# Performance work log

Measured on AMD Instinct MI355X. Metric: run time of the kernel, lower is better.

Reference implementation:

```python
import jax, jax.numpy as jnp
import numpy as np

HIDDEN = 4096
NUM_HEADS = 32
HEAD_DIM = 128          # kv_channels
KV_GROUPS = 2           # multi_query_group_num
ROPE_BASE = 10000.0
ROPE_RATIO = 1.0
QKV_DIM = NUM_HEADS * HEAD_DIM + 2 * KV_GROUPS * HEAD_DIM  # 4608
T = 2048


def _rope_cache(positions):
    # build_rotary_pos with n_elem = rotary_dim//2 = 64 -> 32 frequencies
    n_elem = HEAD_DIM // 2
    theta = 1.0 / (ROPE_BASE ** (jnp.arange(0, n_elem, 2, dtype=jnp.float32) / n_elem))  # [32]
    idx_theta = (positions.astype(jnp.float32) / ROPE_RATIO)[:, None] * theta[None, :]   # [T,32]
    return jnp.cos(idx_theta), jnp.sin(idx_theta)


def _apply_rope(x, cos, sin):
    # x: [T, n_heads, HEAD_DIM]; first rot_dim=2*n_freq dims rotated in interleaved pairs
    t, n, _ = x.shape
    rot_dim = 2 * cos.shape[-1]  # 64
    x_rot, x_pass = x[..., :rot_dim], x[..., rot_dim:]
    xs = x_rot.reshape(t, n, rot_dim // 2, 2)
    c = cos[:, None, :]
    s = sin[:, None, :]
    o0 = xs[..., 0] * c - xs[..., 1] * s
    o1 = xs[..., 1] * c + xs[..., 0] * s
    out = jnp.stack([o0, o1], axis=-1).reshape(t, n, rot_dim)
    return jnp.concatenate([out, x_pass], axis=-1)


def setup_inputs() -> dict:
    key = jax.random.key(0)
    k1, k2, k3, k4 = jax.random.split(key, 4)
    return {
        "positions": jnp.arange(T, dtype=jnp.int64 if jax.config.jax_enable_x64 else jnp.int32),
        "hidden_states": jax.random.normal(k1, (T, HIDDEN), dtype=jnp.float32),
        "w_qkv": jax.random.normal(k2, (HIDDEN, QKV_DIM), dtype=jnp.float32) * 0.02,
        "b_qkv": jax.random.normal(k3, (QKV_DIM,), dtype=jnp.float32) * 0.02,
        "w_dense": jax.random.normal(k4, (HIDDEN, HIDDEN), dtype=jnp.float32) * 0.02,
    }


def reference(positions, hidden_states, w_qkv, b_qkv, w_dense):
    t = hidden_states.shape[0]
    qkv = hidden_states @ w_qkv + b_qkv  # [T, 4608]
    q_sz = NUM_HEADS * HEAD_DIM
    kv_sz = KV_GROUPS * HEAD_DIM
    q = qkv[:, :q_sz].reshape(t, NUM_HEADS, HEAD_DIM)
    k = qkv[:, q_sz:q_sz + kv_sz].reshape(t, KV_GROUPS, HEAD_DIM)
    v = qkv[:, q_sz + kv_sz:].reshape(t, KV_GROUPS, HEAD_DIM)

    cos, sin = _rope_cache(positions)
    q = _apply_rope(q, cos, sin)
    k = _apply_rope(k, cos, sin)

    rep = NUM_HEADS // KV_GROUPS  # MQA: repeat_interleave kv heads
    k = jnp.repeat(k, rep, axis=1)  # [T, NUM_HEADS, HEAD_DIM]
    v = jnp.repeat(v, rep, axis=1)

    scale = HEAD_DIM ** -0.5
    scores = jnp.einsum('qhd,khd->hqk', q, k) * scale  # [H, T, T]
    causal = positions[:, None] >= positions[None, :]
    scores = jnp.where(causal[None, :, :], scores, jnp.float32(-1e9))
    attn = jax.nn.softmax(scores, axis=-1)
    ctx = jnp.einsum('hqk,khd->qhd', attn, v).reshape(t, NUM_HEADS * HEAD_DIM)
    return ctx @ w_dense
```

## Files before the change

kernel.cpp:

```cpp
#include <hip/hip_runtime.h>
#include <hip/hip_bf16.h>

#define T_SEQ 2048
#define HIDDEN_SZ 4096
#define NUM_HEADS 32
#define HEAD_DIM 128
#define KV_GROUPS 2
#define Q_SZ 4096
#define KV_SZ 256
#define QKV_DIM 4608

typedef __attribute__((ext_vector_type(8))) short bf16x8_t;
typedef __attribute__((ext_vector_type(4))) float f32x4_t;

__device__ inline void store_c(float* p, float v) { *p = v; }
__device__ inline void store_c(__hip_bfloat16* p, float v) { *p = __float2bfloat16(v); }

#define GLDS16(gp, lp)                                                                  \
    __builtin_amdgcn_global_load_lds((const __attribute__((address_space(1))) unsigned int*)(gp), \
                                     (__attribute__((address_space(3))) unsigned int*)(lp), 16, 0, 0)

__global__ __launch_bounds__(256) void convert_bf16_kernel(const float* __restrict__ in,
                                                           __hip_bfloat16* __restrict__ out,
                                                           int n) {
    int i = (blockIdx.x * 256 + threadIdx.x) * 4;
    if (i + 3 < n) {
        float4 v = *reinterpret_cast<const float4*>(in + i);
        alignas(8) __hip_bfloat16 tmp[4] = {__float2bfloat16(v.x), __float2bfloat16(v.y),
                                            __float2bfloat16(v.z), __float2bfloat16(v.w)};
        *reinterpret_cast<ushort4*>(out + i) = *reinterpret_cast<const ushort4*>(tmp);
    }
}

__global__ __launch_bounds__(256) void transpose_convert_kernel(const float* __restrict__ in,
                                                                __hip_bfloat16* __restrict__ out,
                                                                int R, int C) {
    __shared__ float tile[64][65];
    const int tx = threadIdx.x & 15;
    const int ty = threadIdx.x >> 4;
    const int c0 = blockIdx.x * 64, r0 = blockIdx.y * 64;
    #pragma unroll
    for (int i = 0; i < 4; ++i) {
        int row = ty + 16 * i;
        float4 v = *reinterpret_cast<const float4*>(&in[(size_t)(r0 + row) * C + c0 + tx * 4]);
        tile[row][tx * 4 + 0] = v.x; tile[row][tx * 4 + 1] = v.y;
        tile[row][tx * 4 + 2] = v.z; tile[row][tx * 4 + 3] = v.w;
    }
    __syncthreads();
    #pragma unroll
    for (int i = 0; i < 4; ++i) {
        int ocol = ty + 16 * i;
        alignas(8) __hip_bfloat16 o[4];
        #pragma unroll
        for (int j = 0; j < 4; ++j) o[j] = __float2bfloat16(tile[tx * 4 + j][ocol]);
        *reinterpret_cast<ushort4*>(&out[(size_t)(c0 + ocol) * R + r0 + tx * 4]) =
            *reinterpret_cast<const ushort4*>(o);
    }
}

template <typename OutT>
__global__ __launch_bounds__(256) void gemm_bf16_kernel(const __hip_bfloat16* __restrict__ A,
                                                        const __hip_bfloat16* __restrict__ BT,
                                                        const float* __restrict__ bias,
                                                        OutT* __restrict__ C,
                                                        int M, int N, int K) {
    constexpr int BM = 128, BN = 128, BK = 32;
    __shared__ __hip_bfloat16 lA[BM * BK];
    __shared__ __hip_bfloat16 lB[BN * BK];
    const int tid = threadIdx.x;
    const int bm = blockIdx.y * BM, bn = blockIdx.x * BN;
    const int wave = tid >> 6, lane = tid & 63;
    const int wr = wave >> 1, wc = wave & 1;
    const int n16 = lane & 15, quad = lane >> 4;
    const int lrow = lane >> 2;
    const int lcol = (lane & 3) * 8;
    f32x4_t acc[4][4] = {};
    for (int kk = 0; kk < K; kk += BK) {
        #pragma unroll
        for (int p = 0; p < 2; ++p) {
            int ca = wave * 2 + p;
            int row = ca * 16 + lrow;
            GLDS16(&A[(size_t)(bm + row) * K + kk + lcol], &lA[ca * 512]);
            GLDS16(&BT[(size_t)(bn + row) * K + kk + lcol], &lB[ca * 512]);
        }
        __syncthreads();
        bf16x8_t af[4], bfr[4];
        #pragma unroll
        for (int i = 0; i < 4; ++i)
            af[i] = *reinterpret_cast<const bf16x8_t*>(&lA[(wr * 64 + i * 16 + n16) * BK + quad * 8]);
        #pragma unroll
        for (int j = 0; j < 4; ++j)
            bfr[j] = *reinterpret_cast<const bf16x8_t*>(&lB[(wc * 64 + j * 16 + n16) * BK + quad * 8]);
        #pragma unroll
        for (int i = 0; i < 4; ++i)
            #pragma unroll
            for (int j = 0; j < 4; ++j)
                acc[i][j] = __builtin_amdgcn_mfma_f32_16x16x32_bf16(af[i], bfr[j], acc[i][j], 0, 0, 0);
        __syncthreads();
    }
    #pragma unroll
    for (int i = 0; i < 4; ++i) {
        #pragma unroll
        for (int j = 0; j < 4; ++j) {
            int col = bn + wc * 64 + j * 16 + n16;
            float bv = bias ? bias[col] : 0.0f;
            #pragma unroll
            for (int r = 0; r < 4; ++r) {
                int row = bm + wr * 64 + i * 16 + quad * 4 + r;
                store_c(&C[(size_t)row * N + col], acc[i][j][r] + bv);
            }
        }
    }
}

__global__ __launch_bounds__(64) void rope_reorg_kernel(const __hip_bfloat16* __restrict__ qkv,
                                                        const int* __restrict__ positions,
                                                        __hip_bfloat16* __restrict__ qo,
                                                        __hip_bfloat16* __restrict__ ko,
                                                        __hip_bfloat16* __restrict__ vTo) {
    const int t = blockIdx.x;
    const int u = blockIdx.y;
    const int tid = threadIdx.x;
    const int d0 = tid * 2, d1 = d0 + 1;
    int col;
    if (u < 32) col = u * HEAD_DIM;
    else if (u < 34) col = Q_SZ + (u - 32) * HEAD_DIM;
    else col = Q_SZ + KV_SZ + (u - 34) * HEAD_DIM;
    float x0 = __bfloat162float(qkv[(size_t)t * QKV_DIM + col + d0]);
    float x1 = __bfloat162float(qkv[(size_t)t * QKV_DIM + col + d1]);
    float o0 = x0, o1 = x1;
    if (u < 34 && tid < 32) {
        float pos = (float)positions[t];
        float theta = exp2f(-(float)tid * 0.4152410118609203f);
        float ang = pos * theta;
        float sn, cs;
        sincosf(ang, &sn, &cs);
        o0 = x0 * cs - x1 * sn;
        o1 = x1 * cs + x0 * sn;
    }
    if (u < 32) {
        constexpr float qscale = 0.08838834764831845f * 1.4426950408889634f;
        __hip_bfloat16* dst = qo + ((size_t)u * T_SEQ + t) * HEAD_DIM;
        dst[d0] = __float2bfloat16(o0 * qscale);
        dst[d1] = __float2bfloat16(o1 * qscale);
    } else if (u < 34) {
        const int gg = u - 32;
        const int kt = t >> 5, kw = t & 31;
        const int c = (kw >> 2) & 1;
        const int n16k = ((kw >> 3) << 2) | (kw & 3);
        const int f = d0 >> 5, quad = (d0 >> 3) & 3, j0 = d0 & 7;
        __hip_bfloat16* dst = ko + (size_t)gg * (T_SEQ * HEAD_DIM) +
                              ((size_t)(((kt * 2 + c) * 4 + f)) << 9) + (quad * 16 + n16k) * 8 + j0;
        dst[0] = __float2bfloat16(o0);
        dst[1] = __float2bfloat16(o1);
    } else {
        const int gg = u - 34;
        const int kt = t >> 5, kw = t & 31;
        const int quad = kw >> 3, j = kw & 7;
        const int dt0 = d0 >> 4, n0 = d0 & 15;
        __hip_bfloat16* dst = vTo + (size_t)gg * (T_SEQ * HEAD_DIM) +
                              ((size_t)(kt * 8 + dt0) << 9) + (quad * 16 + n0) * 8 + j;
        dst[0] = __float2bfloat16(o0);
        dst[8] = __float2bfloat16(o1);
    }
}

__global__ __launch_bounds__(256) void flash_attn_kernel(const __hip_bfloat16* __restrict__ q,
                                                         const __hip_bfloat16* __restrict__ k,
                                                         const __hip_bfloat16* __restrict__ vT,
                                                         __hip_bfloat16* __restrict__ ctx) {
    const int h = blockIdx.y;
    const int g = h >> 4;
    const int wave = threadIdx.x >> 6;
    const int lane = threadIdx.x & 63;
    const int n16 = lane & 15, quad = lane >> 4;
    const int wid = blockIdx.x * 4 + wave;
    const int pr = wid >> 1;
    const int half = wid & 1;
    const int pslot = wave >> 1;
    const __hip_bfloat16* kbase = k + (size_t)g * (T_SEQ * HEAD_DIM) + (size_t)lane * 8;
    const __hip_bfloat16* vbase = vT + (size_t)g * (T_SEQ * HEAD_DIM) + (size_t)lane * 8;

    __shared__ float smO[2][64][33];
    __shared__ float smML[2][64][2];

    for (int pass = 0; pass < 2; ++pass) {
        const int chunk = pass ? (127 - pr) : pr;
        const int qrow0 = chunk * 16;
        const int nt = (chunk >> 1) + 1;
        const int ktA = half ? (nt >> 1) : 0;
        const int ktB = half ? nt : (nt >> 1);
        const int qg = qrow0 + n16;

        const __hip_bfloat16* qrow = q + ((size_t)h * T_SEQ + qg) * HEAD_DIM;
        bf16x8_t qf[4];
        #pragma unroll
        for (int f = 0; f < 4; ++f)
            qf[f] = *reinterpret_cast<const bf16x8_t*>(qrow + f * 32 + quad * 8);

        f32x4_t accO[8] = {};
        float m_ = -1e30f, l_ = 0.0f;

        if (ktA < ktB) {
            bf16x8_t kf[2][4];
            #pragma unroll
            for (int c = 0; c < 2; ++c)
                #pragma unroll
                for (int f = 0; f < 4; ++f)
                    kf[c][f] = *reinterpret_cast<const bf16x8_t*>(
                        kbase + ((size_t)((ktA * 2 + c) * 4 + f) << 9));

            for (int kt = ktA; kt < ktB; ++kt) {
                f32x4_t s[2] = {};
                #pragma unroll
                for (int c = 0; c < 2; ++c)
                    #pragma unroll
                    for (int f = 0; f < 4; ++f)
                        s[c] = __builtin_amdgcn_mfma_f32_16x16x32_bf16(kf[c][f], qf[f], s[c], 0, 0, 0);
                if (kt + 1 < ktB) {
                    int ktn = kt + 1;
                    #pragma unroll
                    for (int c = 0; c < 2; ++c)
                        #pragma unroll
                        for (int f = 0; f < 4; ++f)
                            kf[c][f] = *reinterpret_cast<const bf16x8_t*>(
                                kbase + ((size_t)((ktn * 2 + c) * 4 + f) << 9));
                }
                bf16x8_t vf[8];
                #pragma unroll
                for (int dt = 0; dt < 8; ++dt)
                    vf[dt] = *reinterpret_cast<const bf16x8_t*>(
                        vbase + ((size_t)(kt * 8 + dt) << 9));

                if (kt * 32 + 31 > qrow0) {
                    #pragma unroll
                    for (int c = 0; c < 2; ++c)
                        #pragma unroll
                        for (int r = 0; r < 4; ++r)
                            if (kt * 32 + quad * 8 + c * 4 + r > qg) s[c][r] = -1e30f;
                }
                float xm = fmaxf(fmaxf(fmaxf(s[0][0], s[0][1]), fmaxf(s[0][2], s[0][3])),
                                 fmaxf(fmaxf(s[1][0], s[1][1]), fmaxf(s[1][2], s[1][3])));
                xm = fmaxf(xm, __shfl_xor(xm, 16, 64));
                xm = fmaxf(xm, __shfl_xor(xm, 32, 64));
                float mn = fmaxf(m_, xm);
                float alpha = __builtin_amdgcn_exp2f(m_ - mn);
                m_ = mn;
                float p[2][4];
                #pragma unroll
                for (int c = 0; c < 2; ++c)
                    #pragma unroll
                    for (int r = 0; r < 4; ++r)
                        p[c][r] = __builtin_amdgcn_exp2f(s[c][r] - mn);
                union { bf16x8_t v; __hip_bfloat16 e[8]; } pf;
                #pragma unroll
                for (int c = 0; c < 2; ++c)
                    #pragma unroll
                    for (int r = 0; r < 4; ++r)
                        pf.e[c * 4 + r] = __float2bfloat16(p[c][r]);
                if (__any(alpha < 1.0f)) {
                    #pragma unroll
                    for (int dt = 0; dt < 8; ++dt)
                        #pragma unroll
                        for (int r = 0; r < 4; ++r) accO[dt][r] *= alpha;
                }
                #pragma unroll
                for (int dt = 0; dt < 8; ++dt)
                    accO[dt] = __builtin_amdgcn_mfma_f32_16x16x32_bf16(vf[dt], pf.v, accO[dt], 0, 0, 0);
                float xs = ((p[0][0] + p[0][1]) + (p[0][2] + p[0][3])) +
                           ((p[1][0] + p[1][1]) + (p[1][2] + p[1][3]));
                xs += __shfl_xor(xs, 16, 64);
                xs += __shfl_xor(xs, 32, 64);
                l_ = l_ * alpha + xs;
            }
        }

        if (half) {
            #pragma unroll
            for (int dt = 0; dt < 8; ++dt)
                #pragma unroll
                for (int r = 0; r < 4; ++r) smO[pslot][lane][dt * 4 + r] = accO[dt][r];
            smML[pslot][lane][0] = m_;
            smML[pslot][lane][1] = l_;
        }
        __syncthreads();
        if (!half) {
            float mB = smML[pslot][lane][0], lB = smML[pslot][lane][1];
            float mN = fmaxf(m_, mB);
            float aA = __builtin_amdgcn_exp2f(m_ - mN);
            float aB = __builtin_amdgcn_exp2f(mB - mN);
            float inv = 1.0f / (l_ * aA + lB * aB);
            #pragma unroll
            for (int dt = 0; dt < 8; ++dt) {
                alignas(8) __hip_bfloat16 o[4];
                #pragma unroll
                for (int r = 0; r < 4; ++r)
                    o[r] = __float2bfloat16((accO[dt][r] * aA + smO[pslot][lane][dt * 4 + r] * aB) * inv);
                *reinterpret_cast<ushort4*>(&ctx[(size_t)qg * Q_SZ + h * HEAD_DIM + dt * 16 + quad * 4]) =
                    *reinterpret_cast<const ushort4*>(o);
            }
        }
        __syncthreads();
    }
}

extern "C" void kernel_launch(void* const* d_in, const int* in_sizes, int n_in,
                              void* d_out, int out_size, void* d_ws, size_t ws_size,
                              hipStream_t stream) {
    (void)in_sizes; (void)n_in; (void)out_size; (void)ws_size;
    const int*   positions = (const int*)d_in[0];
    const float* hidden    = (const float*)d_in[1];
    const float* w_qkv     = (const float*)d_in[2];
    const float* b_qkv     = (const float*)d_in[3];
    const float* w_dense   = (const float*)d_in[4];
    float* out = (float*)d_out;

    char* ws = (char*)d_ws;
    __hip_bfloat16* h_bf   = (__hip_bfloat16*)ws; ws += (size_t)T_SEQ * HIDDEN_SZ * 2;
    __hip_bfloat16* wqkvT  = (__hip_bfloat16*)ws; ws += (size_t)QKV_DIM * HIDDEN_SZ * 2;
    __hip_bfloat16* wdT    = (__hip_bfloat16*)ws; ws += (size_t)HIDDEN_SZ * HIDDEN_SZ * 2;
    __hip_bfloat16* qkv_bf = (__hip_bfloat16*)ws; ws += (size_t)T_SEQ * QKV_DIM * 2;
    __hip_bfloat16* q_bf   = (__hip_bfloat16*)ws; ws += (size_t)NUM_HEADS * T_SEQ * HEAD_DIM * 2;
    __hip_bfloat16* k_bf   = (__hip_bfloat16*)ws; ws += (size_t)KV_GROUPS * T_SEQ * HEAD_DIM * 2;
    __hip_bfloat16* vT_bf  = (__hip_bfloat16*)ws; ws += (size_t)KV_GROUPS * HEAD_DIM * T_SEQ * 2;
    __hip_bfloat16* ctx_bf = h_bf;

    convert_bf16_kernel<<<(T_SEQ * HIDDEN_SZ) / (256 * 4), 256, 0, stream>>>(hidden, h_bf, T_SEQ * HIDDEN_SZ);
    transpose_convert_kernel<<<dim3(QKV_DIM / 64, HIDDEN_SZ / 64), 256, 0, stream>>>(w_qkv, wqkvT, HIDDEN_SZ, QKV_DIM);
    transpose_convert_kernel<<<dim3(HIDDEN_SZ / 64, HIDDEN_SZ / 64), 256, 0, stream>>>(w_dense, wdT, HIDDEN_SZ, HIDDEN_SZ);
    gemm_bf16_kernel<__hip_bfloat16><<<dim3(QKV_DIM / 128, T_SEQ / 128), 256, 0, stream>>>(
        h_bf, wqkvT, b_qkv, qkv_bf, T_SEQ, QKV_DIM, HIDDEN_SZ);
    rope_reorg_kernel<<<dim3(T_SEQ, NUM_HEADS + 2 * KV_GROUPS), 64, 0, stream>>>(
        qkv_bf, positions, q_bf, k_bf, vT_bf);
    flash_attn_kernel<<<dim3(32, NUM_HEADS), 256, 0, stream>>>(q_bf, k_bf, vT_bf, ctx_bf);
    gemm_bf16_kernel<float><<<dim3(HIDDEN_SZ / 128, T_SEQ / 128), 256, 0, stream>>>(
        ctx_bf, wdT, nullptr, out, T_SEQ, HIDDEN_SZ, HIDDEN_SZ);
}
```

Baseline: 536.5 us.

## Double-buffer GEMM LDS tiles and swizzle workgroup order

Gives the bf16 GEMM two LDS buffers, so the global-to-LDS load of the next K tile is issued before computing on the current one, with vmcnt waits and barriers instead of two full syncthreads per iteration. It also remaps block IDs with a stride-8 swizzle to change which tiles run concurrently and improve cache reuse. The aim is to hide global load latency behind MFMA work. In exchange LDS use doubles, and correctness depends on the hand-counted vmcnt(4) matching the outstanding loads and on the grid size being divisible by 8.

```diff
diff --git a/kernel.cpp b/kernel.cpp
--- a/kernel.cpp
+++ b/kernel.cpp
@@ -65,39 +65,61 @@
                                                         OutT* __restrict__ C,
                                                         int M, int N, int K) {
     constexpr int BM = 128, BN = 128, BK = 32;
-    __shared__ __hip_bfloat16 lA[BM * BK];
-    __shared__ __hip_bfloat16 lB[BN * BK];
+    __shared__ __hip_bfloat16 lA[2][BM * BK];
+    __shared__ __hip_bfloat16 lB[2][BN * BK];
     const int tid = threadIdx.x;
-    const int bm = blockIdx.y * BM, bn = blockIdx.x * BN;
+    const int nwg = gridDim.x * gridDim.y;
+    const int bid = blockIdx.y * gridDim.x + blockIdx.x;
+    const int swz = (bid & 7) * (nwg >> 3) + (bid >> 3);
+    const int bm = (swz / gridDim.x) * BM, bn = (swz % gridDim.x) * BN;
     const int wave = tid >> 6, lane = tid & 63;
     const int wr = wave >> 1, wc = wave & 1;
     const int n16 = lane & 15, quad = lane >> 4;
     const int lrow = lane >> 2;
     const int lcol = (lane & 3) * 8;
     f32x4_t acc[4][4] = {};
-    for (int kk = 0; kk < K; kk += BK) {
+
+    auto STAGE = [&](int buf, int t) {
+        const int kk = t * BK;
         #pragma unroll
         for (int p = 0; p < 2; ++p) {
             int ca = wave * 2 + p;
             int row = ca * 16 + lrow;
-            GLDS16(&A[(size_t)(bm + row) * K + kk + lcol], &lA[ca * 512]);
-            GLDS16(&BT[(size_t)(bn + row) * K + kk + lcol], &lB[ca * 512]);
-        }
-        __syncthreads();
+            GLDS16(&A[(size_t)(bm + row) * K + kk + lcol], &lA[buf][ca * 512]);
+            GLDS16(&BT[(size_t)(bn + row) * K + kk + lcol], &lB[buf][ca * 512]);
+        }
+    };
+    auto COMPUTE = [&](int buf) {
         bf16x8_t af[4], bfr[4];
         #pragma unroll
         for (int i = 0; i < 4; ++i)
-            af[i] = *reinterpret_cast<const bf16x8_t*>(&lA[(wr * 64 + i * 16 + n16) * BK + quad * 8]);
+            af[i] = *reinterpret_cast<const bf16x8_t*>(&lA[buf][(wr * 64 + i * 16 + n16) * BK + quad * 8]);
         #pragma unroll
         for (int j = 0; j < 4; ++j)
-            bfr[j] = *reinterpret_cast<const bf16x8_t*>(&lB[(wc * 64 + j * 16 + n16) * BK + quad * 8]);
+            bfr[j] = *reinterpret_cast<const bf16x8_t*>(&lB[buf][(wc * 64 + j * 16 + n16) * BK + quad * 8]);
         #pragma unroll
         for (int i = 0; i < 4; ++i)
             #pragma unroll
             for (int j = 0; j < 4; ++j)
                 acc[i][j] = __builtin_amdgcn_mfma_f32_16x16x32_bf16(af[i], bfr[j], acc[i][j], 0, 0, 0);
-        __syncthreads();
-    }
+    };
+
+    const int nt = K / BK;
+    STAGE(0, 0);
+    for (int t = 0; t < nt - 1; ++t) {
+        STAGE((t + 1) & 1, t + 1);
+        asm volatile("s_waitcnt vmcnt(4)" ::: "memory");
+        __builtin_amdgcn_s_barrier();
+        __builtin_amdgcn_sched_barrier(0);
+        COMPUTE(t & 1);
+        __builtin_amdgcn_sched_barrier(0);
+        __builtin_amdgcn_s_barrier();
+    }
+    asm volatile("s_waitcnt vmcnt(0)" ::: "memory");
+    __builtin_amdgcn_s_barrier();
+    __builtin_amdgcn_sched_barrier(0);
+    COMPUTE((nt - 1) & 1);
+
     #pragma unroll
     for (int i = 0; i < 4; ++i) {
         #pragma unroll
```

Result: faster. 514.7 us (-4.1%).

## Rewrite GEMM as 256x256 double-buffered pipelined tile with swizzled LDS

Applied to the files above, without the earlier changes.

Replaces the 128x128 single-buffered GEMM with a 512-thread 256x256x64 kernel. The K loop runs as eight phases that overlap global-to-LDS loads of the next stage with MFMA work on the current buffer, using manual vmcnt waits, barriers and setprio. LDS is XOR-swizzled to avoid bank conflicts, and workgroup IDs are remapped for L2 locality. The rope kernel also packs four tokens per 256-thread block to cut block count. The catch is fewer workgroups: 18x8 for the QKV GEMM and 16x8 for the dense GEMM, which leaves many CUs underused on a large GPU, plus higher register pressure.

```diff
diff --git a/kernel.cpp b/kernel.cpp
--- a/kernel.cpp
+++ b/kernel.cpp
@@ -58,69 +58,135 @@
     }
 }
 
+#define VMC(n) asm volatile("s_waitcnt vmcnt(" #n ")" ::: "memory")
+
+#define GPH(BUF, MH, NH, LDA_EN, LDB_EN, STG, VMS)                              \
+  {                                                                             \
+    if (LDA_EN) {                                                               \
+      _Pragma("unroll") for (int ii = 0; ii < 4; ++ii)                          \
+      _Pragma("unroll") for (int ks = 0; ks < 2; ++ks)                          \
+        a[ii][ks] = LDAf(BUF, MH, ii, ks);                                      \
+    }                                                                           \
+    if (LDB_EN) {                                                               \
+      _Pragma("unroll") for (int jj = 0; jj < 2; ++jj)                          \
+      _Pragma("unroll") for (int ks = 0; ks < 2; ++ks)                          \
+        b[jj][ks] = LDBf(BUF, NH, jj, ks);                                      \
+    }                                                                           \
+    STG;                                                                        \
+    VMS;                                                                        \
+    __builtin_amdgcn_s_barrier();                                               \
+    asm volatile("s_waitcnt lgkmcnt(0)" ::: "memory");                          \
+    __builtin_amdgcn_sched_barrier(0);                                          \
+    __builtin_amdgcn_s_setprio(1);                                              \
+    _Pragma("unroll") for (int ii = 0; ii < 4; ++ii)                            \
+    _Pragma("unroll") for (int jj = 0; jj < 2; ++jj)                            \
+    _Pragma("unroll") for (int ks = 0; ks < 2; ++ks)                            \
+      acc[MH][NH][ii][jj] = __builtin_amdgcn_mfma_f32_16x16x32_bf16(            \
+          a[ii][ks], b[jj][ks], acc[MH][NH][ii][jj], 0, 0, 0);                  \
+    __builtin_amdgcn_s_setprio(0);                                              \
+    __builtin_amdgcn_s_barrier();                                               \
+  }
+
 template <typename OutT>
-__global__ __launch_bounds__(256) void gemm_bf16_kernel(const __hip_bfloat16* __restrict__ A,
-                                                        const __hip_bfloat16* __restrict__ BT,
-                                                        const float* __restrict__ bias,
-                                                        OutT* __restrict__ C,
-                                                        int M, int N, int K) {
-    constexpr int BM = 128, BN = 128, BK = 32;
-    __shared__ __hip_bfloat16 lA[BM * BK];
-    __shared__ __hip_bfloat16 lB[BN * BK];
+__global__ __launch_bounds__(512, 2) void gemm_bf16_kernel(const __hip_bfloat16* __restrict__ A,
+                                                           const __hip_bfloat16* __restrict__ BT,
+                                                           const float* __restrict__ bias,
+                                                           OutT* __restrict__ C,
+                                                           int M, int N, int K) {
+    constexpr int BM = 256, BN = 256, BK = 64;
+    (void)M;
+    __shared__ __hip_bfloat16 sA[2][2][128 * 64];
+    __shared__ __hip_bfloat16 sB[2][2][128 * 64];
     const int tid = threadIdx.x;
-    const int bm = blockIdx.y * BM, bn = blockIdx.x * BN;
+    const int nwg = gridDim.x * gridDim.y;
+    const int bid = blockIdx.y * gridDim.x + blockIdx.x;
+    const int swz = (bid & 7) * (nwg >> 3) + (bid >> 3);
+    const int bm = (swz / gridDim.x) * BM, bn = (swz % gridDim.x) * BN;
     const int wave = tid >> 6, lane = tid & 63;
-    const int wr = wave >> 1, wc = wave & 1;
+    const int wr = wave >> 2, wc = wave & 3;
     const int n16 = lane & 15, quad = lane >> 4;
-    const int lrow = lane >> 2;
-    const int lcol = (lane & 3) * 8;
-    f32x4_t acc[4][4] = {};
-    for (int kk = 0; kk < K; kk += BK) {
+    f32x4_t acc[2][2][4][2] = {};
+    bf16x8_t a[4][2], b[2][2];
+
+    auto STAGE = [&](int isB, int bufb, int half, int kt, const __hip_bfloat16* Mat, int baseRow) {
+        const int kk = kt * BK;
         #pragma unroll
         for (int p = 0; p < 2; ++p) {
-            int ca = wave * 2 + p;
-            int row = ca * 16 + lrow;
-            GLDS16(&A[(size_t)(bm + row) * K + kk + lcol], &lA[ca * 512]);
-            GLDS16(&BT[(size_t)(bn + row) * K + kk + lcol], &lB[ca * 512]);
+            const int u = p * 512 + tid;
+            const int row = u >> 3;
+            const int cs = (u & 7) ^ (row & 7);
+            const __hip_bfloat16* src = Mat + (size_t)(baseRow + row) * K + kk + cs * 8;
+            __hip_bfloat16* dst = (isB ? &sB[bufb][half][0] : &sA[bufb][half][0]) +
+                                  (size_t)(p * 512 + wave * 64) * 8;
+            GLDS16(src, dst);
         }
-        __syncthreads();
-        bf16x8_t af[4], bfr[4];
+    };
+    #define STAGE_A(BUF, HALF, KT) STAGE(0, BUF, HALF, KT, A, bm + (HALF) * 128)
+    #define STAGE_B(BUF, HALF, KT) STAGE(1, BUF, HALF, KT, BT, bn + (HALF) * 128)
+
+    auto LDAf = [&](int bufb, int mh, int iP, int ks) {
+        const int row = wr * 64 + iP * 16 + n16;
+        const int chunk = (ks * 4 + quad) ^ (n16 & 7);
+        return *reinterpret_cast<const bf16x8_t*>(&sA[bufb][mh][row * 64 + chunk * 8]);
+    };
+    auto LDBf = [&](int bufb, int nh, int jP, int ks) {
+        const int row = wc * 32 + jP * 16 + n16;
+        const int chunk = (ks * 4 + quad) ^ (n16 & 7);
+        return *reinterpret_cast<const bf16x8_t*>(&sB[bufb][nh][row * 64 + chunk * 8]);
+    };
+
+    const int NT = K / BK;
+    const int NI = NT / 2;
+    STAGE_A(0, 0, 0); STAGE_B(0, 0, 0); STAGE_B(0, 1, 0); STAGE_A(0, 1, 0);
+    VMC(4);
+    __builtin_amdgcn_s_barrier();
+
+    for (int i = 0; i < NI; ++i) {
+        const int O = 2 * i + 1, E2 = 2 * i + 2;
+        const bool last = (i == NI - 1);
+        GPH(0, 0, 0, true,  true,  STAGE_A(1, 0, O), VMC(4));
+        GPH(0, 0, 1, false, true,  STAGE_B(1, 0, O), VMC(4));
+        GPH(0, 1, 1, true,  false, STAGE_B(1, 1, O), (void)0);
+        GPH(0, 1, 0, false, true,  STAGE_A(1, 1, O), VMC(4));
+        if (!last) {
+            GPH(1, 0, 0, true,  true,  STAGE_A(0, 0, E2), VMC(4));
+            GPH(1, 0, 1, false, true,  STAGE_B(0, 0, E2), VMC(4));
+            GPH(1, 1, 1, true,  false, STAGE_B(0, 1, E2), (void)0);
+            GPH(1, 1, 0, false, true,  STAGE_A(0, 1, E2), VMC(4));
+        } else {
+            GPH(1, 0, 0, true,  true,  (void)0, VMC(2));
+            GPH(1, 0, 1, false, true,  (void)0, VMC(0));
+            GPH(1, 1, 1, true,  false, (void)0, (void)0);
+            GPH(1, 1, 0, false, true,  (void)0, (void)0);
+        }
+    }
+
+    #pragma unroll
+    for (int mh = 0; mh < 2; ++mh)
         #pragma unroll
-        for (int i = 0; i < 4; ++i)
-            af[i] = *reinterpret_cast<const bf16x8_t*>(&lA[(wr * 64 + i * 16 + n16) * BK + quad * 8]);
-        #pragma unroll
-        for (int j = 0; j < 4; ++j)
-            bfr[j] = *reinterpret_cast<const bf16x8_t*>(&lB[(wc * 64 + j * 16 + n16) * BK + quad * 8]);
-        #pragma unroll
-        for (int i = 0; i < 4; ++i)
+        for (int nh = 0; nh < 2; ++nh)
             #pragma unroll
-            for (int j = 0; j < 4; ++j)
-                acc[i][j] = __builtin_amdgcn_mfma_f32_16x16x32_bf16(af[i], bfr[j], acc[i][j], 0, 0, 0);
-        __syncthreads();
-    }
-    #pragma unroll
-    for (int i = 0; i < 4; ++i) {
-        #pragma unroll
-        for (int j = 0; j < 4; ++j) {
-            int col = bn + wc * 64 + j * 16 + n16;
-            float bv = bias ? bias[col] : 0.0f;
-            #pragma unroll
-            for (int r = 0; r < 4; ++r) {
-                int row = bm + wr * 64 + i * 16 + quad * 4 + r;
-                store_c(&C[(size_t)row * N + col], acc[i][j][r] + bv);
-            }
-        }
-    }
-}
-
-__global__ __launch_bounds__(64) void rope_reorg_kernel(const __hip_bfloat16* __restrict__ qkv,
-                                                        const int* __restrict__ positions,
-                                                        __hip_bfloat16* __restrict__ qo,
-                                                        __hip_bfloat16* __restrict__ ko,
-                                                        __hip_bfloat16* __restrict__ vTo) {
-    const int t = blockIdx.x;
+            for (int ii = 0; ii < 4; ++ii)
+                #pragma unroll
+                for (int jj = 0; jj < 2; ++jj) {
+                    const int colg = bn + nh * 128 + wc * 32 + jj * 16 + n16;
+                    const float bv = bias ? bias[colg] : 0.0f;
+                    #pragma unroll
+                    for (int r = 0; r < 4; ++r) {
+                        const int rowg = bm + mh * 128 + wr * 64 + ii * 16 + quad * 4 + r;
+                        store_c(&C[(size_t)rowg * N + colg], acc[mh][nh][ii][jj][r] + bv);
+                    }
+                }
+}
+
+__global__ __launch_bounds__(256) void rope_reorg_kernel(const __hip_bfloat16* __restrict__ qkv,
+                                                         const int* __restrict__ positions,
+                                                         __hip_bfloat16* __restrict__ qo,
+                                                         __hip_bfloat16* __restrict__ ko,
+                                                         __hip_bfloat16* __restrict__ vTo) {
+    const int t = blockIdx.x * 4 + (threadIdx.x >> 6);
     const int u = blockIdx.y;
-    const int tid = threadIdx.x;
+    const int tid = threadIdx.x & 63;
     const int d0 = tid * 2, d1 = d0 + 1;
     int col;
     if (u < 32) col = u * HEAD_DIM;
@@ -328,11 +394,11 @@
     convert_bf16_kernel<<<(T_SEQ * HIDDEN_SZ) / (256 * 4), 256, 0, stream>>>(hidden, h_bf, T_SEQ * HIDDEN_SZ);
     transpose_convert_kernel<<<dim3(QKV_DIM / 64, HIDDEN_SZ / 64), 256, 0, stream>>>(w_qkv, wqkvT, HIDDEN_SZ, QKV_DIM);
     transpose_convert_kernel<<<dim3(HIDDEN_SZ / 64, HIDDEN_SZ / 64), 256, 0, stream>>>(w_dense, wdT, HIDDEN_SZ, HIDDEN_SZ);
-    gemm_bf16_kernel<__hip_bfloat16><<<dim3(QKV_DIM / 128, T_SEQ / 128), 256, 0, stream>>>(
+    gemm_bf16_kernel<__hip_bfloat16><<<dim3(QKV_DIM / 256, T_SEQ / 256), 512, 0, stream>>>(
         h_bf, wqkvT, b_qkv, qkv_bf, T_SEQ, QKV_DIM, HIDDEN_SZ);
-    rope_reorg_kernel<<<dim3(T_SEQ, NUM_HEADS + 2 * KV_GROUPS), 64, 0, stream>>>(
+    rope_reorg_kernel<<<dim3(T_SEQ / 4, NUM_HEADS + 2 * KV_GROUPS), 256, 0, stream>>>(
         qkv_bf, positions, q_bf, k_bf, vT_bf);
     flash_attn_kernel<<<dim3(32, NUM_HEADS), 256, 0, stream>>>(q_bf, k_bf, vT_bf, ctx_bf);
-    gemm_bf16_kernel<float><<<dim3(HIDDEN_SZ / 128, T_SEQ / 128), 256, 0, stream>>>(
+    gemm_bf16_kernel<float><<<dim3(HIDDEN_SZ / 256, T_SEQ / 256), 512, 0, stream>>>(
         ctx_bf, wdT, nullptr, out, T_SEQ, HIDDEN_SZ, HIDDEN_SZ);
 }
```

Result: slower. 1.161 ms (+116.4%).
